# Kernel optimization log

Measured on AMD Instinct MI355X. Metric: run time of the kernel, lower is better.

The kernel has to match this reference:

```python
import jax, jax.numpy as jnp
import numpy as np

B, S, N, F = 4, 256, 128, 64
D = 128          # d_model == 2*F so encoder/decoder dims agree
NH = 4           # hard-coded num_heads in both MHA blocks


def _linear(x, w, b):
    # torch nn.Linear: y = x @ W.T + b, W: (out, in)
    return x @ w.T + b


def _mha(q, k, v, w_in, b_in, w_out, b_out, nh):
    # torch nn.MultiheadAttention (batch_first=True) with packed in_proj
    bq, sq, e = q.shape
    hd = e // nh
    qp = _linear(q, w_in[:e], b_in[:e])
    kp = _linear(k, w_in[e:2 * e], b_in[e:2 * e])
    vp = _linear(v, w_in[2 * e:], b_in[2 * e:])
    qh = qp.reshape(bq, sq, nh, hd)
    kh = kp.reshape(bq, k.shape[1], nh, hd)
    vh = vp.reshape(bq, v.shape[1], nh, hd)
    scores = jnp.einsum('bqhd,bkhd->bhqk', qh, kh) / np.sqrt(hd).astype(np.float32)
    attn = jax.nn.softmax(scores, axis=-1)
    out = jnp.einsum('bhqk,bkhd->bqhd', attn, vh).reshape(bq, sq, e)
    return _linear(out, w_out, b_out)


def _pos_enc(s, d):
    pos = jnp.arange(s, dtype=jnp.float32)[:, None]
    div = jnp.exp(jnp.arange(0, d, 2, dtype=jnp.float32) * (-np.log(10000.0) / d))
    pe = jnp.zeros((s, d), dtype=jnp.float32)
    pe = pe.at[:, 0::2].set(jnp.sin(pos * div))
    pe = pe.at[:, 1::2].set(jnp.cos(pos * div))
    return pe


def _haar_decouple(x):
    # exact vectorized pywt haar dwt + single-branch idwt (even seq_len)
    b, s, n, f = x.shape
    pairs = x.reshape(b, s // 2, 2, n, f)
    avg = (pairs[:, :, 0] + pairs[:, :, 1]) * 0.5  # idwt(cA, None) value
    dif = (pairs[:, :, 0] - pairs[:, :, 1]) * 0.5  # idwt(None, cD) value
    x_l = jnp.stack([avg, avg], axis=2).reshape(b, s, n, f)
    x_h = jnp.stack([dif, -dif], axis=2).reshape(b, s, n, f)
    return x_l, x_h


def setup_inputs() -> dict:
    key = jax.random.key(0)
    ks = jax.random.split(key, 32)
    p = lambda i, shp: jax.random.normal(ks[i], shp, jnp.float32) * 0.02
    return {
        'x': jax.random.normal(ks[0], (B, S, N, F), jnp.float32),
        'ts': jax.random.randint(ks[1], (B, S), 0, 252),
        'ta_w_in': p(2, (3 * D, D)), 'ta_b_in': p(3, (3 * D,)),
        'ta_w_out': p(4, (D, D)), 'ta_b_out': p(5, (D,)),
        'conv_w': p(6, (D, 2 * F, 3)), 'conv_b': p(7, (D,)),
        'pl_w': p(8, (D, D)), 'pl_b': p(9, (D,)),
        'ph_w': p(10, (D, D)), 'ph_b': p(11, (D,)),
        'as_w_in': p(12, (3 * D, D)), 'as_b_in': p(13, (3 * D,)),
        'as_w_out': p(14, (D, D)), 'as_b_out': p(15, (D,)),
        'ac_w_in': p(16, (3 * D, D)), 'ac_b_in': p(17, (3 * D,)),
        'ac_w_out': p(18, (D, D)), 'ac_b_out': p(19, (D,)),
        'rl_w': p(20, (1, D)), 'rl_b': p(21, (1,)),
        'cl_w': p(22, (2, D)), 'cl_b': p(23, (2,)),
        'rf_w': p(24, (1, D)), 'rf_b': p(25, (1,)),
        'cf_w': p(26, (2, D)), 'cf_b': p(27, (2,)),
    }


def reference(x, ts, ta_w_in, ta_b_in, ta_w_out, ta_b_out, conv_w, conv_b,
              pl_w, pl_b, ph_w, ph_b, as_w_in, as_b_in, as_w_out, as_b_out,
              ac_w_in, ac_b_in, ac_w_out, ac_b_out, rl_w, rl_b, cl_w, cl_b,
              rf_w, rf_b, cf_w, cf_b):
    b, s, n, f = x.shape
    # --- DecouplingFlowLayer (vectorized haar) ---
    x_l, x_h = _haar_decouple(x)
    xl_cat = jnp.concatenate([x, x_l], axis=-1)  # (b,s,n,2f)
    xh_cat = jnp.concatenate([x, x_h], axis=-1)
    e = 2 * f
    # --- DualFrequencyEncoder ---
    pe = _pos_enc(s, e)
    xl_flat = xl_cat.transpose(0, 2, 1, 3).reshape(b * n, s, e) + pe
    x_tatt = _mha(xl_flat, xl_flat, xl_flat, ta_w_in, ta_b_in, ta_w_out, ta_b_out, NH)
    x_l_gat = x_tatt.reshape(b, s, n, e)  # faithful raw .view() as in torch
    xh_flat = xh_cat.transpose(0, 2, 3, 1).reshape(b * n, e, s)
    conv = jax.lax.conv_general_dilated(
        xh_flat, conv_w, window_strides=(1,), padding=[(2, 2)],
        rhs_dilation=(2,), dimension_numbers=('NCH', 'OIH', 'NCH'))
    conv = jax.nn.relu(conv + conv_b[None, :, None])
    x_h_gat = conv.reshape(b, n, -1, s).transpose(0, 3, 1, 2)  # (b,s,n,D)
    d = x_h_gat.shape[-1]
    # ts -> time_embedding is computed then discarded in the original forward: dead code
    # --- DualFrequencyFusionDecoder ---
    y_l = x_l_gat.reshape(b * n, s, d)
    y_h = x_h_gat.reshape(b * n, s, d)
    q_l = _linear(y_l, pl_w, pl_b)
    k_h = _linear(y_h, ph_w, ph_b)
    y_l2 = _linear(q_l, pl_w, pl_b)  # predictor_l applied twice, as in torch
    lreg = _linear(y_l2, rl_w, rl_b).reshape(b, s, n)
    lcla = jax.nn.softmax(_linear(y_l2, cl_w, cl_b), axis=-1).reshape(b, s, n, 2)
    a_self = _mha(q_l, q_l, q_l, as_w_in, as_b_in, as_w_out, as_b_out, NH)
    a_cross = _mha(q_l, k_h, k_h, ac_w_in, ac_b_in, ac_w_out, ac_b_out, NH)
    fused = (a_self + a_cross).reshape(b, s, n, d)
    reg = _linear(fused, rf_w, rf_b)[..., 0]
    cla = jax.nn.softmax(_linear(fused, cf_w, cf_b), axis=-1)
    return reg, cla, lreg, lcla
```

## Files before the change

### kernel.cpp

```cpp
#include <hip/hip_runtime.h>
#include <hip/hip_bf16.h>

typedef __attribute__((ext_vector_type(8))) short short8v;
typedef __attribute__((ext_vector_type(4))) short short4v;
typedef __attribute__((ext_vector_type(4))) float f32x4;
typedef __hip_bfloat16 bh;

constexpr long SF_ELEMS = 131072L * 128;
#define MFMA16(a, b, c) __builtin_amdgcn_mfma_f32_16x16x32_bf16((a), (b), (c), 0, 0, 0)

__device__ __forceinline__ short bh_bits(float x) {
  bh h = __float2bfloat16(x);
  return *reinterpret_cast<short*>(&h);
}


__global__ __launch_bounds__(256) void sf_wcvt(const float* __restrict__ s0, const float* __restrict__ s1,
                                               const float* __restrict__ s2, const float* __restrict__ s3,
                                               const float* __restrict__ s4, const float* __restrict__ s5,
                                               const float* __restrict__ s6, const float* __restrict__ s7,
                                               const float* __restrict__ cw,
                                               bh* __restrict__ dst) {
  int i = blockIdx.x * 256 + threadIdx.x;
  float v;
  if      (i <  49152) v = s0[i];
  else if (i <  65536) v = s1[i - 49152];
  else if (i <  81920) v = s2[i - 65536];
  else if (i <  98304) v = s3[i - 81920];
  else if (i < 147456) v = s4[i - 98304];
  else if (i < 163840) v = s5[i - 147456];
  else if (i < 212992) v = s6[i - 163840];
  else if (i < 229376) v = s7[i - 212992];
  else if (i < 278528) {
    int j = i - 229376;
    int tap = j >> 14, rem = j & 16383;
    v = cw[rem * 3 + tap];
  } else return;
  dst[i] = __float2bfloat16(v);
}

__global__ __launch_bounds__(256) void sf_pe(float* __restrict__ pe) {
  int i = blockIdx.x * 256 + threadIdx.x;
  int e = i & 127, s = i >> 7;
  int ii = e >> 1;
  float dv = expf(-0.0719557945041855f * (float)(2 * ii));
  float ang = (float)s * dv;
  pe[i] = (e & 1) ? cosf(ang) : sinf(ang);
}

__global__ __launch_bounds__(256) void sf_build_z(const float* __restrict__ x,
                                                  const float* __restrict__ pe,
                                                  bh* __restrict__ z) {
  long i = (long)blockIdx.x * 256 + threadIdx.x;
  if (i >= SF_ELEMS) return;
  int e = (int)(i & 127);
  int s = (int)((i >> 7) & 255);
  int r = (int)(i >> 15);
  int b = r >> 7, stk = r & 127;
  float val;
  if (e < 64) {
    val = x[(((long)b * 256 + s) * 128 + stk) * 64 + e];
  } else {
    int f = e - 64;
    int t2 = s >> 1;
    float a0 = x[(((long)b * 256 + 2 * t2) * 128 + stk) * 64 + f];
    float a1 = x[(((long)b * 256 + 2 * t2 + 1) * 128 + stk) * 64 + f];
    val = 0.5f * (a0 + a1);
  }
  z[i] = __float2bfloat16(val + pe[s * 128 + e]);
}

__global__ __launch_bounds__(256) void sf_build_xh(const float* __restrict__ x,
                                                   bh* __restrict__ xh) {
  long i = (long)blockIdx.x * 256 + threadIdx.x;
  if (i >= SF_ELEMS) return;
  int ic = (int)(i & 127);
  int s = (int)((i >> 7) & 255);
  int r = (int)(i >> 15);
  int b = r >> 7, stk = r & 127;
  float val;
  if (ic < 64) {
    val = x[(((long)b * 256 + s) * 128 + stk) * 64 + ic];
  } else {
    int f = ic - 64;
    int t2 = s >> 1;
    float a0 = x[(((long)b * 256 + 2 * t2) * 128 + stk) * 64 + f];
    float a1 = x[(((long)b * 256 + 2 * t2 + 1) * 128 + stk) * 64 + f];
    float d = 0.5f * (a0 - a1);
    val = (s & 1) ? -d : d;
  }
  xh[i] = __float2bfloat16(val);
}

template <bool ACC>
__global__ __launch_bounds__(256) void sf_lin(const bh* __restrict__ X,
                                              const bh* __restrict__ Wb,
                                              const float* __restrict__ bias,
                                              const bh* __restrict__ Prev,
                                              bh* __restrict__ Y) {
  __shared__ bh Lw[4][32][140];
  const int t = threadIdx.x, lane = t & 63, w = t >> 6;
  const int lr = lane & 15, lg = lane >> 4;
  const long R0 = (long)blockIdx.x * 128 + w * 32;
  const f32x4 z4 = {0.f, 0.f, 0.f, 0.f};
  short8v a[2][4];
#pragma unroll
  for (int ks = 0; ks < 4; ++ks) {
    a[0][ks] = *reinterpret_cast<const short8v*>(X + (R0 + lr) * 128 + ks * 32 + lg * 8);
    a[1][ks] = *reinterpret_cast<const short8v*>(X + (R0 + 16 + lr) * 128 + ks * 32 + lg * 8);
  }
  f32x4 acc[2][8];
#pragma unroll
  for (int m = 0; m < 2; ++m)
#pragma unroll
    for (int n = 0; n < 8; ++n) acc[m][n] = z4;
#pragma unroll
  for (int ks = 0; ks < 4; ++ks) {
#pragma unroll
    for (int n = 0; n < 8; ++n) {
      short8v b = *reinterpret_cast<const short8v*>(Wb + (long)(n * 16 + lr) * 128 + ks * 32 + lg * 8);
      acc[0][n] = MFMA16(a[0][ks], b, acc[0][n]);
      acc[1][n] = MFMA16(a[1][ks], b, acc[1][n]);
    }
  }
#pragma unroll
  for (int n = 0; n < 8; ++n) {
    float bv = bias[n * 16 + lr];
#pragma unroll
    for (int m = 0; m < 2; ++m)
#pragma unroll
      for (int r = 0; r < 4; ++r)
        Lw[w][m * 16 + 4 * lg + r][n * 16 + lr] = __float2bfloat16(acc[m][n][r] + bv);
  }
  __syncthreads();
#pragma unroll
  for (int c = 0; c < 8; ++c) {
    int row_l = c * 4 + lg;
    short8v v = *reinterpret_cast<const short8v*>(&Lw[w][row_l][lr * 8]);
    if (ACC) {
      short8v pv = *reinterpret_cast<const short8v*>(Prev + (R0 + row_l) * 128 + lr * 8);
      bh* va = reinterpret_cast<bh*>(&v);
      const bh* pa = reinterpret_cast<const bh*>(&pv);
#pragma unroll
      for (int j = 0; j < 8; ++j)
        va[j] = __float2bfloat16(__bfloat162float(va[j]) + __bfloat162float(pa[j]));
    }
    *reinterpret_cast<short8v*>(Y + (R0 + row_l) * 128 + lr * 8) = v;
  }
}

__global__ __launch_bounds__(256) void sf_convm(const bh* __restrict__ Xh,
                                                const bh* __restrict__ Wr,
                                                const float* __restrict__ bias,
                                                bh* __restrict__ Yh) {
  __shared__ bh Lw[4][32][140];
  const int t = threadIdx.x, lane = t & 63, w = t >> 6;
  const int lr = lane & 15, lg = lane >> 4;
  const int bnc = blockIdx.x >> 1;
  const int half = blockIdx.x & 1;
  const int b = bnc >> 7, stk = bnc & 127;
  const int R0 = half * 128 + w * 32;
  const f32x4 z4 = {0.f, 0.f, 0.f, 0.f};
  const short8v zf = {0, 0, 0, 0, 0, 0, 0, 0};
  f32x4 acc[2][8];
#pragma unroll
  for (int m = 0; m < 2; ++m)
#pragma unroll
    for (int n = 0; n < 8; ++n) acc[m][n] = z4;
#pragma unroll
  for (int tap = 0; tap < 3; ++tap) {
    const int shift = 2 * tap - 2;
#pragma unroll
    for (int ks = 0; ks < 4; ++ks) {
      int s0 = R0 + lr + shift;
      int s1 = s0 + 16;
      short8v a0 = zf, a1 = zf;
      if ((unsigned)s0 < 256u)
        a0 = *reinterpret_cast<const short8v*>(Xh + ((long)bnc * 256 + s0) * 128 + ks * 32 + lg * 8);
      if ((unsigned)s1 < 256u)
        a1 = *reinterpret_cast<const short8v*>(Xh + ((long)bnc * 256 + s1) * 128 + ks * 32 + lg * 8);
#pragma unroll
      for (int n = 0; n < 8; ++n) {
        short8v bb = *reinterpret_cast<const short8v*>(Wr + (long)tap * 16384 + (long)(n * 16 + lr) * 128 + ks * 32 + lg * 8);
        acc[0][n] = MFMA16(a0, bb, acc[0][n]);
        acc[1][n] = MFMA16(a1, bb, acc[1][n]);
      }
    }
  }
#pragma unroll
  for (int n = 0; n < 8; ++n) {
    float bv = bias[n * 16 + lr];
#pragma unroll
    for (int m = 0; m < 2; ++m)
#pragma unroll
      for (int r = 0; r < 4; ++r)
        Lw[w][m * 16 + 4 * lg + r][n * 16 + lr] = __float2bfloat16(fmaxf(acc[m][n][r] + bv, 0.f));
  }
  __syncthreads();
#pragma unroll
  for (int c = 0; c < 8; ++c) {
    int row_l = c * 4 + lg;
    int sc = R0 + row_l;
    int rp = b * 128 + (sc >> 1);
    int sp = ((sc & 1) << 7) + stk;
    short8v v = *reinterpret_cast<const short8v*>(&Lw[w][row_l][lr * 8]);
    *reinterpret_cast<short8v*>(Yh + ((long)rp * 256 + sp) * 128 + lr * 8) = v;
  }
}

__global__ __launch_bounds__(256) void sf_attnp(const bh* Qsrc, const bh* KVsrc,
                                                const bh* __restrict__ Win,
                                                const float* __restrict__ bin,
                                                bh* __restrict__ O) {
  __shared__ bh Ks[256][36];
  __shared__ bh Vt[32][260];
  __shared__ bh Qs[4][64][36];
  __shared__ bh Pl[4][16][72];
  const int t = threadIdx.x, lane = t & 63, w = t >> 6;
  const int lr = lane & 15, lg = lane >> 4;
  const int bn = blockIdx.x >> 2, h = blockIdx.x & 3;
  const long R0 = (long)bn * 256;
  const int ch = h * 32;
  const f32x4 z4 = {0.f, 0.f, 0.f, 0.f};
  {
    short8v wq[2][4];
#pragma unroll
    for (int n = 0; n < 2; ++n)
#pragma unroll
      for (int ks = 0; ks < 4; ++ks)
        wq[n][ks] = *reinterpret_cast<const short8v*>(Win + (long)(ch + n * 16 + lr) * 128 + ks * 32 + lg * 8);
#pragma unroll
    for (int m2 = 0; m2 < 4; ++m2) {
      short8v asv[4];
#pragma unroll
      for (int ks = 0; ks < 4; ++ks)
        asv[ks] = *reinterpret_cast<const short8v*>(Qsrc + (R0 + w * 64 + m2 * 16 + lr) * 128 + ks * 32 + lg * 8);
#pragma unroll
      for (int n = 0; n < 2; ++n) {
        f32x4 acc = z4;
#pragma unroll
        for (int ks = 0; ks < 4; ++ks) acc = MFMA16(asv[ks], wq[n][ks], acc);
        float bb = bin[ch + n * 16 + lr];
#pragma unroll
        for (int r = 0; r < 4; ++r)
          Qs[w][m2 * 16 + 4 * lg + r][n * 16 + lr] = __float2bfloat16(acc[r] + bb);
      }
    }
  }
  {
    short8v wk[2][4], wv[2][4];
#pragma unroll
    for (int n = 0; n < 2; ++n)
#pragma unroll
      for (int ks = 0; ks < 4; ++ks) {
        wk[n][ks] = *reinterpret_cast<const short8v*>(Win + (long)(128 + ch + n * 16 + lr) * 128 + ks * 32 + lg * 8);
        wv[n][ks] = *reinterpret_cast<const short8v*>(Win + (long)(256 + ch + n * 16 + lr) * 128 + ks * 32 + lg * 8);
      }
#pragma unroll
    for (int m2 = 0; m2 < 4; ++m2) {
      short8v asv[4];
#pragma unroll
      for (int ks = 0; ks < 4; ++ks)
        asv[ks] = *reinterpret_cast<const short8v*>(KVsrc + (R0 + w * 64 + m2 * 16 + lr) * 128 + ks * 32 + lg * 8);
#pragma unroll
      for (int n = 0; n < 2; ++n) {
        f32x4 ak = z4, av = z4;
#pragma unroll
        for (int ks = 0; ks < 4; ++ks) {
          ak = MFMA16(asv[ks], wk[n][ks], ak);
          av = MFMA16(asv[ks], wv[n][ks], av);
        }
        float bk = bin[128 + ch + n * 16 + lr];
        float bv = bin[256 + ch + n * 16 + lr];
#pragma unroll
        for (int r = 0; r < 4; ++r)
          Ks[w * 64 + m2 * 16 + 4 * lg + r][n * 16 + lr] = __float2bfloat16(ak[r] + bk);
        short4v pv;
#pragma unroll
        for (int r = 0; r < 4; ++r) pv[r] = bh_bits(av[r] + bv);
        *reinterpret_cast<short4v*>(&Vt[n * 16 + lr][w * 64 + m2 * 16 + 4 * lg]) = pv;
      }
    }
  }
  __syncthreads();
  const float sc = 0.17677669529663687f;
  short8v aq[4];
#pragma unroll
  for (int mt = 0; mt < 4; ++mt)
    aq[mt] = *reinterpret_cast<const short8v*>(&Qs[w][mt * 16 + lr][lg * 8]);
  f32x4 Oacc[4][2];
  float psum[4] = {0.f, 0.f, 0.f, 0.f};
#pragma unroll
  for (int mt = 0; mt < 4; ++mt) { Oacc[mt][0] = z4; Oacc[mt][1] = z4; }
#pragma unroll
  for (int kt = 0; kt < 4; ++kt) {
    short8v bvf[2][2];
#pragma unroll
    for (int dt = 0; dt < 2; ++dt)
#pragma unroll
      for (int ks = 0; ks < 2; ++ks)
        bvf[dt][ks] = *reinterpret_cast<const short8v*>(&Vt[dt * 16 + lr][kt * 64 + ks * 32 + lg * 8]);
#pragma unroll
    for (int mt = 0; mt < 4; ++mt) {
      f32x4 st[4];
#pragma unroll
      for (int nt = 0; nt < 4; ++nt) {
        short8v bk = *reinterpret_cast<const short8v*>(&Ks[kt * 64 + nt * 16 + lr][lg * 8]);
        st[nt] = MFMA16(bk, aq[mt], z4);
      }
      float ps = 0.f;
#pragma unroll
      for (int nt = 0; nt < 4; ++nt) {
        float p0 = __expf(st[nt][0] * sc);
        float p1 = __expf(st[nt][1] * sc);
        float p2 = __expf(st[nt][2] * sc);
        float p3 = __expf(st[nt][3] * sc);
        ps += (p0 + p1) + (p2 + p3);
        short4v pk;
        pk[0] = bh_bits(p0); pk[1] = bh_bits(p1); pk[2] = bh_bits(p2); pk[3] = bh_bits(p3);
        *reinterpret_cast<short4v*>(&Pl[w][lr][nt * 16 + 4 * lg]) = pk;
      }
      psum[mt] += ps;
#pragma unroll
      for (int ks = 0; ks < 2; ++ks) {
        short8v ap = *reinterpret_cast<const short8v*>(&Pl[w][lr][ks * 32 + lg * 8]);
        Oacc[mt][0] = MFMA16(ap, bvf[0][ks], Oacc[mt][0]);
        Oacc[mt][1] = MFMA16(ap, bvf[1][ks], Oacc[mt][1]);
      }
    }
  }
#pragma unroll
  for (int mt = 0; mt < 4; ++mt) {
    float ps = psum[mt];
    ps += __shfl_xor(ps, 16, 64);
    ps += __shfl_xor(ps, 32, 64);
    float inv = 1.f / ps;
#pragma unroll
    for (int r = 0; r < 4; ++r) {
      float invr = __shfl(inv, 4 * lg + r, 64);
      long row = R0 + w * 64 + mt * 16 + 4 * lg + r;
      O[row * 128 + ch + lr]      = __float2bfloat16(Oacc[mt][0][r] * invr);
      O[row * 128 + ch + 16 + lr] = __float2bfloat16(Oacc[mt][1][r] * invr);
    }
  }
}

__global__ __launch_bounds__(256) void sf_heads(const bh* __restrict__ X,
                                                const float* __restrict__ rw,
                                                const float* __restrict__ rb,
                                                const float* __restrict__ cw,
                                                const float* __restrict__ cb,
                                                float* __restrict__ out,
                                                long off_reg, long off_cla) {
  __shared__ float w0[128], w1[128], w2[128];
  const int t = threadIdx.x;
  if (t < 128) { w0[t] = rw[t]; w1[t] = cw[t]; w2[t] = cw[128 + t]; }
  __syncthreads();
  long row = (long)blockIdx.x * 256 + t;
  const bh* xr = X + row * 128;
  float d0 = 0.f, d1 = 0.f, d2 = 0.f;
#pragma unroll 4
  for (int j = 0; j < 128; j += 8) {
    short8v v8 = *reinterpret_cast<const short8v*>(xr + j);
    const bh* vv = reinterpret_cast<const bh*>(&v8);
#pragma unroll
    for (int k = 0; k < 8; ++k) {
      float f = __bfloat162float(vv[k]);
      d0 = fmaf(f, w0[j + k], d0);
      d1 = fmaf(f, w1[j + k], d1);
      d2 = fmaf(f, w2[j + k], d2);
    }
  }
  d0 += rb[0]; d1 += cb[0]; d2 += cb[1];
  float mx = fmaxf(d1, d2);
  float e1 = expf(d1 - mx), e2 = expf(d2 - mx);
  float inv = 1.f / (e1 + e2);
  out[off_reg + row] = d0;
  out[off_cla + row * 2] = e1 * inv;
  out[off_cla + row * 2 + 1] = e2 * inv;
}

extern "C" void kernel_launch(void* const* d_in, const int* in_sizes, int n_in,
                              void* d_out, int out_size, void* d_ws, size_t ws_size,
                              hipStream_t stream) {
  (void)in_sizes; (void)n_in; (void)out_size; (void)ws_size;
  const float* x       = (const float*)d_in[0];
  const float* ta_w_in = (const float*)d_in[2];
  const float* ta_b_in = (const float*)d_in[3];
  const float* ta_w_o  = (const float*)d_in[4];
  const float* ta_b_o  = (const float*)d_in[5];
  const float* conv_w  = (const float*)d_in[6];
  const float* conv_b  = (const float*)d_in[7];
  const float* pl_w    = (const float*)d_in[8];
  const float* pl_b    = (const float*)d_in[9];
  const float* ph_w    = (const float*)d_in[10];
  const float* ph_b    = (const float*)d_in[11];
  const float* as_w_in = (const float*)d_in[12];
  const float* as_b_in = (const float*)d_in[13];
  const float* as_w_o  = (const float*)d_in[14];
  const float* as_b_o  = (const float*)d_in[15];
  const float* ac_w_in = (const float*)d_in[16];
  const float* ac_b_in = (const float*)d_in[17];
  const float* ac_w_o  = (const float*)d_in[18];
  const float* ac_b_o  = (const float*)d_in[19];
  const float* rl_w    = (const float*)d_in[20];
  const float* rl_b    = (const float*)d_in[21];
  const float* cl_w    = (const float*)d_in[22];
  const float* cl_b    = (const float*)d_in[23];
  const float* rf_w    = (const float*)d_in[24];
  const float* rf_b    = (const float*)d_in[25];
  const float* cf_w    = (const float*)d_in[26];
  const float* cf_b    = (const float*)d_in[27];
  float* out = (float*)d_out;

  bh* S0 = (bh*)d_ws;
  bh* S1 = S0 + SF_ELEMS;
  bh* S2 = S1 + SF_ELEMS;
  bh* S3 = S2 + SF_ELEMS;
  bh* S4 = S3 + SF_ELEMS;
  bh* A  = S4 + SF_ELEMS;
  float* PE = (float*)(A + 278528);

  dim3 blk(256);
  const int GZ = (int)(SF_ELEMS / 256);
  const int GL = 1024;
  const bh* np = nullptr;

  sf_wcvt<<<1088, blk, 0, stream>>>(ta_w_in, ta_w_o, pl_w, ph_w, ac_w_in, ac_w_o,
                                    as_w_in, as_w_o, conv_w, A);
  sf_pe<<<128, blk, 0, stream>>>(PE);

  sf_build_z<<<GZ, blk, 0, stream>>>(x, PE, S0);
  sf_attnp<<<2048, blk, 0, stream>>>(S0, S0, A, ta_b_in, S1);
  sf_lin<false><<<GL, blk, 0, stream>>>(S1, A + 49152, ta_b_o, np, S2);
  sf_build_xh<<<GZ, blk, 0, stream>>>(x, S3);
  sf_convm<<<1024, blk, 0, stream>>>(S3, A + 229376, conv_b, S4);

  sf_lin<false><<<GL, blk, 0, stream>>>(S4, A + 81920, ph_b, np, S0);
  sf_lin<false><<<GL, blk, 0, stream>>>(S2, A + 65536, pl_b, np, S1);
  sf_lin<false><<<GL, blk, 0, stream>>>(S1, A + 65536, pl_b, np, S3);
  sf_heads<<<512, blk, 0, stream>>>(S3, rl_w, rl_b, cl_w, cl_b, out, 393216L, 524288L);

  sf_attnp<<<2048, blk, 0, stream>>>(S1, S0, A + 98304, ac_b_in, S2);
  sf_lin<false><<<GL, blk, 0, stream>>>(S2, A + 147456, ac_b_o, np, S3);

  sf_attnp<<<2048, blk, 0, stream>>>(S1, S1, A + 163840, as_b_in, S4);
  sf_lin<true><<<GL, blk, 0, stream>>>(S4, A + 212992, as_b_o, S3, S2);

  sf_heads<<<512, blk, 0, stream>>>(S2, rf_w, rf_b, cf_w, cf_b, out, 0L, 131072L);
}
```

Measured before the change: 519.9 us.

## Fuse encoder out-proj, predictor chain and heads; merge input builders

Merges the two input-building kernels into one pass over x, so the strided reads are shared. Fuses the encoder out-projection, the two predictor_l linears and the low-frequency heads into one kernel. It also fuses the final self-attention out-projection, the residual add and the output heads. The attention softmax scale is folded into Q, with exp2 replacing exp. The __syncthreads calls in the per-wave LDS staging are removed, which trims launches and intermediate global round trips. In exchange the fused kernels keep more live registers, and the exp2 rewrite depends on the folded scale being correct.

```diff
diff --git a/kernel.cpp b/kernel.cpp
--- a/kernel.cpp
+++ b/kernel.cpp
@@ -48,55 +48,36 @@
   pe[i] = (e & 1) ? cosf(ang) : sinf(ang);
 }
 
-__global__ __launch_bounds__(256) void sf_build_z(const float* __restrict__ x,
+__global__ __launch_bounds__(256) void sf_buildzx(const float* __restrict__ x,
                                                   const float* __restrict__ pe,
-                                                  bh* __restrict__ z) {
+                                                  bh* __restrict__ z,
+                                                  bh* __restrict__ xh) {
   long i = (long)blockIdx.x * 256 + threadIdx.x;
   if (i >= SF_ELEMS) return;
   int e = (int)(i & 127);
   int s = (int)((i >> 7) & 255);
   int r = (int)(i >> 15);
   int b = r >> 7, stk = r & 127;
-  float val;
+  float zv, hv;
   if (e < 64) {
-    val = x[(((long)b * 256 + s) * 128 + stk) * 64 + e];
+    float val = x[(((long)b * 256 + s) * 128 + stk) * 64 + e];
+    zv = val; hv = val;
   } else {
     int f = e - 64;
     int t2 = s >> 1;
     float a0 = x[(((long)b * 256 + 2 * t2) * 128 + stk) * 64 + f];
     float a1 = x[(((long)b * 256 + 2 * t2 + 1) * 128 + stk) * 64 + f];
-    val = 0.5f * (a0 + a1);
-  }
-  z[i] = __float2bfloat16(val + pe[s * 128 + e]);
-}
-
-__global__ __launch_bounds__(256) void sf_build_xh(const float* __restrict__ x,
-                                                   bh* __restrict__ xh) {
-  long i = (long)blockIdx.x * 256 + threadIdx.x;
-  if (i >= SF_ELEMS) return;
-  int ic = (int)(i & 127);
-  int s = (int)((i >> 7) & 255);
-  int r = (int)(i >> 15);
-  int b = r >> 7, stk = r & 127;
-  float val;
-  if (ic < 64) {
-    val = x[(((long)b * 256 + s) * 128 + stk) * 64 + ic];
-  } else {
-    int f = ic - 64;
-    int t2 = s >> 1;
-    float a0 = x[(((long)b * 256 + 2 * t2) * 128 + stk) * 64 + f];
-    float a1 = x[(((long)b * 256 + 2 * t2 + 1) * 128 + stk) * 64 + f];
+    zv = 0.5f * (a0 + a1);
     float d = 0.5f * (a0 - a1);
-    val = (s & 1) ? -d : d;
-  }
-  xh[i] = __float2bfloat16(val);
-}
-
-template <bool ACC>
+    hv = (s & 1) ? -d : d;
+  }
+  z[i] = __float2bfloat16(zv + pe[s * 128 + e]);
+  xh[i] = __float2bfloat16(hv);
+}
+
 __global__ __launch_bounds__(256) void sf_lin(const bh* __restrict__ X,
                                               const bh* __restrict__ Wb,
                                               const float* __restrict__ bias,
-                                              const bh* __restrict__ Prev,
                                               bh* __restrict__ Y) {
   __shared__ bh Lw[4][32][140];
   const int t = threadIdx.x, lane = t & 63, w = t >> 6;
@@ -132,19 +113,10 @@
       for (int r = 0; r < 4; ++r)
         Lw[w][m * 16 + 4 * lg + r][n * 16 + lr] = __float2bfloat16(acc[m][n][r] + bv);
   }
-  __syncthreads();
 #pragma unroll
   for (int c = 0; c < 8; ++c) {
     int row_l = c * 4 + lg;
     short8v v = *reinterpret_cast<const short8v*>(&Lw[w][row_l][lr * 8]);
-    if (ACC) {
-      short8v pv = *reinterpret_cast<const short8v*>(Prev + (R0 + row_l) * 128 + lr * 8);
-      bh* va = reinterpret_cast<bh*>(&v);
-      const bh* pa = reinterpret_cast<const bh*>(&pv);
-#pragma unroll
-      for (int j = 0; j < 8; ++j)
-        va[j] = __float2bfloat16(__bfloat162float(va[j]) + __bfloat162float(pa[j]));
-    }
     *reinterpret_cast<short8v*>(Y + (R0 + row_l) * 128 + lr * 8) = v;
   }
 }
@@ -196,7 +168,6 @@
       for (int r = 0; r < 4; ++r)
         Lw[w][m * 16 + 4 * lg + r][n * 16 + lr] = __float2bfloat16(fmaxf(acc[m][n][r] + bv, 0.f));
   }
-  __syncthreads();
 #pragma unroll
   for (int c = 0; c < 8; ++c) {
     int row_l = c * 4 + lg;
@@ -214,14 +185,14 @@
                                                 bh* __restrict__ O) {
   __shared__ bh Ks[256][36];
   __shared__ bh Vt[32][260];
-  __shared__ bh Qs[4][64][36];
-  __shared__ bh Pl[4][16][72];
+  __shared__ bh QP[4][64][36];
   const int t = threadIdx.x, lane = t & 63, w = t >> 6;
   const int lr = lane & 15, lg = lane >> 4;
   const int bn = blockIdx.x >> 2, h = blockIdx.x & 3;
   const long R0 = (long)bn * 256;
   const int ch = h * 32;
   const f32x4 z4 = {0.f, 0.f, 0.f, 0.f};
+  const float SC2 = 0.2550351f;
   {
     short8v wq[2][4];
 #pragma unroll
@@ -243,7 +214,7 @@
         float bb = bin[ch + n * 16 + lr];
 #pragma unroll
         for (int r = 0; r < 4; ++r)
-          Qs[w][m2 * 16 + 4 * lg + r][n * 16 + lr] = __float2bfloat16(acc[r] + bb);
+          QP[w][m2 * 16 + 4 * lg + r][n * 16 + lr] = __float2bfloat16((acc[r] + bb) * SC2);
       }
     }
   }
@@ -283,11 +254,11 @@
     }
   }
   __syncthreads();
-  const float sc = 0.17677669529663687f;
   short8v aq[4];
 #pragma unroll
   for (int mt = 0; mt < 4; ++mt)
-    aq[mt] = *reinterpret_cast<const short8v*>(&Qs[w][mt * 16 + lr][lg * 8]);
+    aq[mt] = *reinterpret_cast<const short8v*>(&QP[w][mt * 16 + lr][lg * 8]);
+  bh* plp = &QP[w][0][0];
   f32x4 Oacc[4][2];
   float psum[4] = {0.f, 0.f, 0.f, 0.f};
 #pragma unroll
@@ -311,19 +282,19 @@
       float ps = 0.f;
 #pragma unroll
       for (int nt = 0; nt < 4; ++nt) {
-        float p0 = __expf(st[nt][0] * sc);
-        float p1 = __expf(st[nt][1] * sc);
-        float p2 = __expf(st[nt][2] * sc);
-        float p3 = __expf(st[nt][3] * sc);
+        float p0 = exp2f(st[nt][0]);
+        float p1 = exp2f(st[nt][1]);
+        float p2 = exp2f(st[nt][2]);
+        float p3 = exp2f(st[nt][3]);
         ps += (p0 + p1) + (p2 + p3);
         short4v pk;
         pk[0] = bh_bits(p0); pk[1] = bh_bits(p1); pk[2] = bh_bits(p2); pk[3] = bh_bits(p3);
-        *reinterpret_cast<short4v*>(&Pl[w][lr][nt * 16 + 4 * lg]) = pk;
+        *reinterpret_cast<short4v*>(&plp[lr * 72 + nt * 16 + 4 * lg]) = pk;
       }
       psum[mt] += ps;
 #pragma unroll
       for (int ks = 0; ks < 2; ++ks) {
-        short8v ap = *reinterpret_cast<const short8v*>(&Pl[w][lr][ks * 32 + lg * 8]);
+        short8v ap = *reinterpret_cast<const short8v*>(&plp[lr * 72 + ks * 32 + lg * 8]);
         Oacc[mt][0] = MFMA16(ap, bvf[0][ks], Oacc[mt][0]);
         Oacc[mt][1] = MFMA16(ap, bvf[1][ks], Oacc[mt][1]);
       }
@@ -345,39 +316,198 @@
   }
 }
 
-__global__ __launch_bounds__(256) void sf_heads(const bh* __restrict__ X,
-                                                const float* __restrict__ rw,
-                                                const float* __restrict__ rb,
-                                                const float* __restrict__ cw,
-                                                const float* __restrict__ cb,
-                                                float* __restrict__ out,
-                                                long off_reg, long off_cla) {
-  __shared__ float w0[128], w1[128], w2[128];
-  const int t = threadIdx.x;
-  if (t < 128) { w0[t] = rw[t]; w1[t] = cw[t]; w2[t] = cw[128 + t]; }
+__global__ __launch_bounds__(256) void sf_encdec(const bh* __restrict__ X,
+                                                 const bh* __restrict__ Wo, const float* __restrict__ bo,
+                                                 const bh* __restrict__ Wpl, const float* __restrict__ bpl,
+                                                 const float* __restrict__ rw, const float* __restrict__ rb,
+                                                 const float* __restrict__ cw, const float* __restrict__ cb,
+                                                 bh* __restrict__ Yq, float* __restrict__ out,
+                                                 long off_reg, long off_cla) {
+  __shared__ bh Lw[4][32][140];
+  __shared__ float hw[3][128];
+  const int t = threadIdx.x, lane = t & 63, w = t >> 6;
+  const int lr = lane & 15, lg = lane >> 4;
+  const long R0 = (long)blockIdx.x * 128 + w * 32;
+  const f32x4 z4 = {0.f, 0.f, 0.f, 0.f};
+  if (t < 128) { hw[0][t] = rw[t]; hw[1][t] = cw[t]; hw[2][t] = cw[128 + t]; }
+  {
+    short8v a[2][4];
+#pragma unroll
+    for (int ks = 0; ks < 4; ++ks) {
+      a[0][ks] = *reinterpret_cast<const short8v*>(X + (R0 + lr) * 128 + ks * 32 + lg * 8);
+      a[1][ks] = *reinterpret_cast<const short8v*>(X + (R0 + 16 + lr) * 128 + ks * 32 + lg * 8);
+    }
+    f32x4 acc[2][8];
+#pragma unroll
+    for (int m = 0; m < 2; ++m)
+#pragma unroll
+      for (int n = 0; n < 8; ++n) acc[m][n] = z4;
+#pragma unroll
+    for (int ks = 0; ks < 4; ++ks)
+#pragma unroll
+      for (int n = 0; n < 8; ++n) {
+        short8v b = *reinterpret_cast<const short8v*>(Wo + (long)(n * 16 + lr) * 128 + ks * 32 + lg * 8);
+        acc[0][n] = MFMA16(a[0][ks], b, acc[0][n]);
+        acc[1][n] = MFMA16(a[1][ks], b, acc[1][n]);
+      }
+#pragma unroll
+    for (int n = 0; n < 8; ++n) {
+      float bv = bo[n * 16 + lr];
+#pragma unroll
+      for (int m = 0; m < 2; ++m)
+#pragma unroll
+        for (int r = 0; r < 4; ++r)
+          Lw[w][m * 16 + 4 * lg + r][n * 16 + lr] = __float2bfloat16(acc[m][n][r] + bv);
+    }
+  }
+#pragma unroll
+  for (int stage = 0; stage < 2; ++stage) {
+    short8v a[2][4];
+#pragma unroll
+    for (int ks = 0; ks < 4; ++ks) {
+      a[0][ks] = *reinterpret_cast<const short8v*>(&Lw[w][lr][ks * 32 + lg * 8]);
+      a[1][ks] = *reinterpret_cast<const short8v*>(&Lw[w][16 + lr][ks * 32 + lg * 8]);
+    }
+    f32x4 acc[2][8];
+#pragma unroll
+    for (int m = 0; m < 2; ++m)
+#pragma unroll
+      for (int n = 0; n < 8; ++n) acc[m][n] = z4;
+#pragma unroll
+    for (int ks = 0; ks < 4; ++ks)
+#pragma unroll
+      for (int n = 0; n < 8; ++n) {
+        short8v b = *reinterpret_cast<const short8v*>(Wpl + (long)(n * 16 + lr) * 128 + ks * 32 + lg * 8);
+        acc[0][n] = MFMA16(a[0][ks], b, acc[0][n]);
+        acc[1][n] = MFMA16(a[1][ks], b, acc[1][n]);
+      }
+#pragma unroll
+    for (int n = 0; n < 8; ++n) {
+      float bv = bpl[n * 16 + lr];
+#pragma unroll
+      for (int m = 0; m < 2; ++m)
+#pragma unroll
+        for (int r = 0; r < 4; ++r)
+          Lw[w][m * 16 + 4 * lg + r][n * 16 + lr] = __float2bfloat16(acc[m][n][r] + bv);
+    }
+    if (stage == 0) {
+#pragma unroll
+      for (int c = 0; c < 8; ++c) {
+        int row_l = c * 4 + lg;
+        short8v v = *reinterpret_cast<const short8v*>(&Lw[w][row_l][lr * 8]);
+        *reinterpret_cast<short8v*>(Yq + (R0 + row_l) * 128 + lr * 8) = v;
+      }
+    }
+  }
   __syncthreads();
-  long row = (long)blockIdx.x * 256 + t;
-  const bh* xr = X + row * 128;
-  float d0 = 0.f, d1 = 0.f, d2 = 0.f;
-#pragma unroll 4
-  for (int j = 0; j < 128; j += 8) {
-    short8v v8 = *reinterpret_cast<const short8v*>(xr + j);
-    const bh* vv = reinterpret_cast<const bh*>(&v8);
-#pragma unroll
-    for (int k = 0; k < 8; ++k) {
-      float f = __bfloat162float(vv[k]);
-      d0 = fmaf(f, w0[j + k], d0);
-      d1 = fmaf(f, w1[j + k], d1);
-      d2 = fmaf(f, w2[j + k], d2);
-    }
-  }
-  d0 += rb[0]; d1 += cb[0]; d2 += cb[1];
-  float mx = fmaxf(d1, d2);
-  float e1 = expf(d1 - mx), e2 = expf(d2 - mx);
-  float inv = 1.f / (e1 + e2);
-  out[off_reg + row] = d0;
-  out[off_cla + row * 2] = e1 * inv;
-  out[off_cla + row * 2 + 1] = e2 * inv;
+  {
+    const int rr = lane >> 1, hh = lane & 1;
+    float d0 = 0.f, d1 = 0.f, d2 = 0.f;
+#pragma unroll
+    for (int j = 0; j < 8; ++j) {
+      short8v v8 = *reinterpret_cast<const short8v*>(&Lw[w][rr][hh * 64 + j * 8]);
+      const bh* vv = reinterpret_cast<const bh*>(&v8);
+#pragma unroll
+      for (int k = 0; k < 8; ++k) {
+        float f = __bfloat162float(vv[k]);
+        int c = hh * 64 + j * 8 + k;
+        d0 = fmaf(f, hw[0][c], d0);
+        d1 = fmaf(f, hw[1][c], d1);
+        d2 = fmaf(f, hw[2][c], d2);
+      }
+    }
+    d0 += __shfl_xor(d0, 1, 64);
+    d1 += __shfl_xor(d1, 1, 64);
+    d2 += __shfl_xor(d2, 1, 64);
+    if (hh == 0) {
+      long row = R0 + rr;
+      d0 += rb[0]; d1 += cb[0]; d2 += cb[1];
+      float mx = fmaxf(d1, d2);
+      float e1 = __expf(d1 - mx), e2 = __expf(d2 - mx);
+      float inv = 1.f / (e1 + e2);
+      out[off_reg + row] = d0;
+      out[off_cla + row * 2] = e1 * inv;
+      out[off_cla + row * 2 + 1] = e2 * inv;
+    }
+  }
+}
+
+__global__ __launch_bounds__(256) void sf_fin(const bh* __restrict__ X,
+                                              const bh* __restrict__ Was, const float* __restrict__ bo,
+                                              const bh* __restrict__ Prev,
+                                              const float* __restrict__ rw, const float* __restrict__ rb,
+                                              const float* __restrict__ cw, const float* __restrict__ cb,
+                                              float* __restrict__ out, long off_reg, long off_cla) {
+  __shared__ bh Lw[4][32][140];
+  __shared__ float hw[3][128];
+  const int t = threadIdx.x, lane = t & 63, w = t >> 6;
+  const int lr = lane & 15, lg = lane >> 4;
+  const long R0 = (long)blockIdx.x * 128 + w * 32;
+  const f32x4 z4 = {0.f, 0.f, 0.f, 0.f};
+  if (t < 128) { hw[0][t] = rw[t]; hw[1][t] = cw[t]; hw[2][t] = cw[128 + t]; }
+  {
+    short8v a[2][4];
+#pragma unroll
+    for (int ks = 0; ks < 4; ++ks) {
+      a[0][ks] = *reinterpret_cast<const short8v*>(X + (R0 + lr) * 128 + ks * 32 + lg * 8);
+      a[1][ks] = *reinterpret_cast<const short8v*>(X + (R0 + 16 + lr) * 128 + ks * 32 + lg * 8);
+    }
+    f32x4 acc[2][8];
+#pragma unroll
+    for (int m = 0; m < 2; ++m)
+#pragma unroll
+      for (int n = 0; n < 8; ++n) acc[m][n] = z4;
+#pragma unroll
+    for (int ks = 0; ks < 4; ++ks)
+#pragma unroll
+      for (int n = 0; n < 8; ++n) {
+        short8v b = *reinterpret_cast<const short8v*>(Was + (long)(n * 16 + lr) * 128 + ks * 32 + lg * 8);
+        acc[0][n] = MFMA16(a[0][ks], b, acc[0][n]);
+        acc[1][n] = MFMA16(a[1][ks], b, acc[1][n]);
+      }
+#pragma unroll
+    for (int n = 0; n < 8; ++n) {
+      float bv = bo[n * 16 + lr];
+#pragma unroll
+      for (int m = 0; m < 2; ++m)
+#pragma unroll
+        for (int r = 0; r < 4; ++r)
+          Lw[w][m * 16 + 4 * lg + r][n * 16 + lr] = __float2bfloat16(acc[m][n][r] + bv);
+    }
+  }
+  __syncthreads();
+  {
+    const int rr = lane >> 1, hh = lane & 1;
+    float d0 = 0.f, d1 = 0.f, d2 = 0.f;
+#pragma unroll
+    for (int j = 0; j < 8; ++j) {
+      short8v v8 = *reinterpret_cast<const short8v*>(&Lw[w][rr][hh * 64 + j * 8]);
+      short8v p8 = *reinterpret_cast<const short8v*>(Prev + (R0 + rr) * 128 + hh * 64 + j * 8);
+      const bh* vv = reinterpret_cast<const bh*>(&v8);
+      const bh* pp = reinterpret_cast<const bh*>(&p8);
+#pragma unroll
+      for (int k = 0; k < 8; ++k) {
+        float f = __bfloat162float(vv[k]) + __bfloat162float(pp[k]);
+        int c = hh * 64 + j * 8 + k;
+        d0 = fmaf(f, hw[0][c], d0);
+        d1 = fmaf(f, hw[1][c], d1);
+        d2 = fmaf(f, hw[2][c], d2);
+      }
+    }
+    d0 += __shfl_xor(d0, 1, 64);
+    d1 += __shfl_xor(d1, 1, 64);
+    d2 += __shfl_xor(d2, 1, 64);
+    if (hh == 0) {
+      long row = R0 + rr;
+      d0 += rb[0]; d1 += cb[0]; d2 += cb[1];
+      float mx = fmaxf(d1, d2);
+      float e1 = __expf(d1 - mx), e2 = __expf(d2 - mx);
+      float inv = 1.f / (e1 + e2);
+      out[off_reg + row] = d0;
+      out[off_cla + row * 2] = e1 * inv;
+      out[off_cla + row * 2 + 1] = e2 * inv;
+    }
+  }
 }
 
 extern "C" void kernel_launch(void* const* d_in, const int* in_sizes, int n_in,
@@ -424,28 +554,23 @@
   dim3 blk(256);
   const int GZ = (int)(SF_ELEMS / 256);
   const int GL = 1024;
-  const bh* np = nullptr;
 
   sf_wcvt<<<1088, blk, 0, stream>>>(ta_w_in, ta_w_o, pl_w, ph_w, ac_w_in, ac_w_o,
                                     as_w_in, as_w_o, conv_w, A);
   sf_pe<<<128, blk, 0, stream>>>(PE);
 
-  sf_build_z<<<GZ, blk, 0, stream>>>(x, PE, S0);
+  sf_buildzx<<<GZ, blk, 0, stream>>>(x, PE, S0, S3);
   sf_attnp<<<2048, blk, 0, stream>>>(S0, S0, A, ta_b_in, S1);
-  sf_lin<false><<<GL, blk, 0, stream>>>(S1, A + 49152, ta_b_o, np, S2);
-  sf_build_xh<<<GZ, blk, 0, stream>>>(x, S3);
+  sf_encdec<<<GL, blk, 0, stream>>>(S1, A + 49152, ta_b_o, A + 65536, pl_b,
+                                    rl_w, rl_b, cl_w, cl_b, S2, out,
+                                    393216L, 524288L);
   sf_convm<<<1024, blk, 0, stream>>>(S3, A + 229376, conv_b, S4);
-
-  sf_lin<false><<<GL, blk, 0, stream>>>(S4, A + 81920, ph_b, np, S0);
-  sf_lin<false><<<GL, blk, 0, stream>>>(S2, A + 65536, pl_b, np, S1);
-  sf_lin<false><<<GL, blk, 0, stream>>>(S1, A + 65536, pl_b, np, S3);
-  sf_heads<<<512, blk, 0, stream>>>(S3, rl_w, rl_b, cl_w, cl_b, out, 393216L, 524288L);
-
-  sf_attnp<<<2048, blk, 0, stream>>>(S1, S0, A + 98304, ac_b_in, S2);
-  sf_lin<false><<<GL, blk, 0, stream>>>(S2, A + 147456, ac_b_o, np, S3);
-
-  sf_attnp<<<2048, blk, 0, stream>>>(S1, S1, A + 163840, as_b_in, S4);
-  sf_lin<true><<<GL, blk, 0, stream>>>(S4, A + 212992, as_b_o, S3, S2);
-
-  sf_heads<<<512, blk, 0, stream>>>(S2, rf_w, rf_b, cf_w, cf_b, out, 0L, 131072L);
-}
+  sf_lin<<<GL, blk, 0, stream>>>(S4, A + 81920, ph_b, S0);
+
+  sf_attnp<<<2048, blk, 0, stream>>>(S2, S0, A + 98304, ac_b_in, S3);
+  sf_lin<<<GL, blk, 0, stream>>>(S3, A + 147456, ac_b_o, S4);
+
+  sf_attnp<<<2048, blk, 0, stream>>>(S2, S2, A + 163840, as_b_in, S1);
+  sf_fin<<<GL, blk, 0, stream>>>(S1, A + 212992, as_b_o, S4,
+                                 rf_w, rf_b, cf_w, cf_b, out, 0L, 131072L);
+}
```

Result: faster. 471.2 us (median of 2 runs) (-9.4%).
